# Kernel optimization log

Hardware: AMD Instinct MI355X
Metric: run time of the kernel (lower is better)

## Reference

```python
import jax, jax.numpy as jnp
import numpy as np

B, D, H, E, K = 4096, 1024, 4096, 8, 2

def setup_inputs() -> dict:
    key = jax.random.key(0)
    ks = jax.random.split(key, 6)
    return {
        "x_modality": jax.random.normal(ks[0], (B, D), dtype=jnp.float32),
        "expert_indices": jax.random.randint(ks[1], (B, K), 0, E, dtype=jnp.int32),
        "hard_weights": jax.random.uniform(ks[2], (B, K), dtype=jnp.float32),
        "w1": jax.random.normal(ks[3], (E, D, H), dtype=jnp.float32) * (1.0 / np.sqrt(D)),
        "b1": jnp.zeros((E, H), dtype=jnp.float32),
        "w2": jax.random.normal(ks[4], (E, H, D), dtype=jnp.float32) * (1.0 / np.sqrt(H)),
        "b2": jnp.zeros((E, D), dtype=jnp.float32),
    }

def reference(x_modality, expert_indices, hard_weights, w1, b1, w2, b2):
    b = x_modality.shape[0]
    # Per-token gate per expert: sum of hard_weights over top_k slots routed to that expert.
    gates = jnp.zeros((b, E), dtype=x_modality.dtype)
    gates = gates.at[jnp.arange(b)[:, None], expert_indices].add(hard_weights)  # [b, E]
    # Dense expert compute (small fixed E), then gated combine.
    h = jax.nn.gelu(jnp.einsum("bd,edh->ebh", x_modality, w1) + b1[:, None, :], approximate=False)
    y = jnp.einsum("ebh,ehd->ebd", h, w2) + b2[:, None, :]  # [E, b, D]
    return jnp.einsum("be,ebd->bd", gates, y)
```

## Files before the change

### kernel.cpp

```cpp
#include <hip/hip_runtime.h>
#include <hip/hip_bf16.h>
#include <math.h>

#define NB 4096
#define ND 1024
#define NH 4096
#define NE 8
#define NKK 2
#define NROWS (NB*NKK)
#define MAXT2 40

typedef __attribute__((ext_vector_type(8))) short short8;
typedef __attribute__((ext_vector_type(4))) float f32x4;

__device__ __forceinline__ void gload_lds16(const void* g, void* l) {
    __builtin_amdgcn_global_load_lds(
        (const __attribute__((address_space(1))) unsigned int*)g,
        (__attribute__((address_space(3))) unsigned int*)l, 16, 0, 0);
}

__device__ __forceinline__ unsigned short f2bf(float f) {
    __hip_bfloat16 h = __float2bfloat16(f);
    return *reinterpret_cast<unsigned short*>(&h);
}

__device__ __forceinline__ float fast_gelu(float x) {
    float xs  = x * 0.70710678118654752f;
    float axs = fabsf(xs);
    float t   = __builtin_amdgcn_rcpf(1.0f + 0.3275911f * axs);
    float p   = t * (0.254829592f + t * (-0.284496736f + t * (1.421413741f +
                t * (-1.453152027f + t * 1.061405429f))));
    float e   = __expf(-xs * xs);
    float erf_abs = 1.0f - p * e;
    float erf = copysignf(erf_abs, x);
    return 0.5f * x * (1.0f + erf);
}


__global__ void k_transpose_cvt(const float* __restrict__ in, __hip_bfloat16* __restrict__ out,
                                int R, int C) {
    __shared__ float tile[64][68];
    const size_t ebase = (size_t)blockIdx.z * R * C;
    const int r0 = blockIdx.y * 64, c0 = blockIdx.x * 64;
    const int t = threadIdx.x;
    const int lr = t >> 4, lc4 = (t & 15) * 4;
    #pragma unroll
    for (int i = 0; i < 4; ++i) {
        int r = lr + i * 16;
        float4 v = *reinterpret_cast<const float4*>(&in[ebase + (size_t)(r0 + r) * C + (c0 + lc4)]);
        *reinterpret_cast<float4*>(&tile[r][lc4]) = v;
    }
    __syncthreads();
    const int q = t & 15, cw = t >> 4;
    #pragma unroll
    for (int i = 0; i < 4; ++i) {
        int cc = cw + i * 16;
        ushort4 v;
        v.x = f2bf(tile[q*4+0][cc]);
        v.y = f2bf(tile[q*4+1][cc]);
        v.z = f2bf(tile[q*4+2][cc]);
        v.w = f2bf(tile[q*4+3][cc]);
        *reinterpret_cast<ushort4*>(&out[ebase + (size_t)(c0 + cc) * R + (r0 + q*4)]) = v;
    }
}


__global__ void k_route_count(const int* __restrict__ idx, int* cnt) {
    int b = blockIdx.x * 256 + threadIdx.x;
    if (b < NB) {
        atomicAdd(&cnt[idx[2*b]], 1);
        atomicAdd(&cnt[idx[2*b+1]], 1);
    }
}

__global__ void k_route_scan(const int* __restrict__ cnt, int* offs, int* cursor,
                             int* tile_e, int* tile_row, int* ntiles) {
    if (threadIdx.x == 0) {
        int s = 0, t = 0;
        for (int e = 0; e < NE; ++e) {
            offs[e] = s; cursor[e] = s;
            for (int r = 0; r < cnt[e]; r += 256) {
                tile_e[t] = e; tile_row[t] = s + r; ++t;
            }
            s += cnt[e];
        }
        offs[NE] = s;
        *ntiles = t;
    }
}

__global__ void k_route_fill(const int* __restrict__ idx, const float* __restrict__ hw,
                             int* cursor, int* tok, float* gw) {
    int b = blockIdx.x * 256 + threadIdx.x;
    if (b < NB) {
        #pragma unroll
        for (int k = 0; k < NKK; ++k) {
            int e = idx[2*b + k];
            int p = atomicAdd(&cursor[e], 1);
            tok[p] = b;
            gw[p]  = hw[2*b + k];
        }
    }
}

__global__ void k_gather_cvt(const float* __restrict__ x, const int* __restrict__ tok,
                             __hip_bfloat16* __restrict__ Ag) {
    const int row = blockIdx.x;
    const float4 v = reinterpret_cast<const float4*>(x + (size_t)tok[row] * ND)[threadIdx.x];
    ushort4 u; u.x = f2bf(v.x); u.y = f2bf(v.y); u.z = f2bf(v.z); u.w = f2bf(v.w);
    reinterpret_cast<ushort4*>(Ag + (size_t)row * ND)[threadIdx.x] = u;
}


template<int STAGE>
__global__ __launch_bounds__(512, 2) void moe_gemm(
    const __hip_bfloat16* __restrict__ Asrc,
    const __hip_bfloat16* __restrict__ Bt,
    const float* __restrict__ bias,
    __hip_bfloat16* __restrict__ Hout,
    float* __restrict__ Out,
    const int* __restrict__ offs,
    const int* __restrict__ tok,
    const float* __restrict__ gw,
    const int* __restrict__ tile_e,
    const int* __restrict__ tile_row,
    const int* __restrict__ ntiles)
{
    constexpr int N   = (STAGE == 1) ? NH : ND;
    constexpr int K   = (STAGE == 1) ? ND : NH;
    constexpr int BN  = (STAGE == 1) ? 256 : 128;
    constexpr int KT  = (STAGE == 1) ? 16 : 32;
    constexpr int NI  = BN / 64;
    constexpr int BR  = (BN * 64) / (512 * 8);
    constexpr int ASZ = 256 * 64;
    constexpr int BUF = ASZ + BN * 64;

    extern __shared__ __hip_bfloat16 smem[];

    const int bid = blockIdx.x;
    const int xcd = bid & 7;
    const int c   = bid >> 3;
    const int tile = (xcd >> 1) * 10 + (c >> 3);
    const int sub  = c & 7;
    if (tile >= *ntiles) return;

    int nt, kbase;
    if (STAGE == 1) { nt = (xcd & 1) * 8 + sub; kbase = 0; }
    else            { nt = sub;                 kbase = (xcd & 1) * (NH / 2); }

    const int e = tile_e[tile];
    const int rowbase = tile_row[tile];
    const int end = offs[e + 1];

    const int tid = threadIdx.x;
    const int w = tid >> 6, l = tid & 63;
    const int srow = tid >> 3;
    const int schunk = (tid & 7) ^ (srow & 7);

    const __hip_bfloat16* aptr[4];
    #pragma unroll
    for (int r = 0; r < 4; ++r) {
        int re = rowbase + srow + r * 64; if (re > end - 1) re = end - 1;
        aptr[r] = Asrc + (size_t)re * K + kbase + schunk * 8;
    }
    const __hip_bfloat16* bptr[BR];
    #pragma unroll
    for (int r = 0; r < BR; ++r)
        bptr[r] = Bt + ((size_t)e * N + (size_t)(nt * BN + srow + r * 64)) * K + kbase + schunk * 8;

    const int wm  = (w >> 2) * 128;
    const int wn  = (w & 3) * (BN / 4);
    const int l15 = l & 15, l4 = l >> 4;

    const int cs[2] = { ((l4) ^ (l15 & 7)) * 16, ((4 + l4) ^ (l15 & 7)) * 16 };
    const int abase = (wm + l15) * 128;
    const int bbase = (wn + l15) * 128;

    f32x4 acc[8][NI];
    #pragma unroll
    for (int mi = 0; mi < 8; ++mi)
        #pragma unroll
        for (int ni = 0; ni < NI; ++ni) acc[mi][ni] = (f32x4){0.f, 0.f, 0.f, 0.f};

    auto stage_t = [&](int b, int kt) {
        __hip_bfloat16* da = smem + b * BUF;
        __hip_bfloat16* db = da + ASZ;
        #pragma unroll
        for (int r = 0; r < 4; ++r)  gload_lds16(aptr[r] + kt * 64, da + tid * 8 + r * 4096);
        #pragma unroll
        for (int r = 0; r < BR; ++r) gload_lds16(bptr[r] + kt * 64, db + tid * 8 + r * 4096);
    };

    stage_t(0, 0);
    __syncthreads();

    int cur = 0;
    #pragma unroll 1
    for (int kt = 0; kt < KT; ++kt) {
        if (kt + 1 < KT) stage_t(cur ^ 1, kt + 1);
        const char* sa = (const char*)(smem + cur * BUF);
        const char* sb = (const char*)(smem + cur * BUF + ASZ);
        __builtin_amdgcn_s_setprio(1);
        #pragma unroll
        for (int ks = 0; ks < 2; ++ks) {
            short8 af[8], bfv[NI];
            #pragma unroll
            for (int mi = 0; mi < 8; ++mi)
                af[mi] = *(const short8*)(sa + abase + mi * 2048 + cs[ks]);
            #pragma unroll
            for (int ni = 0; ni < NI; ++ni)
                bfv[ni] = *(const short8*)(sb + bbase + ni * 2048 + cs[ks]);
            #pragma unroll
            for (int mi = 0; mi < 8; ++mi)
                #pragma unroll
                for (int ni = 0; ni < NI; ++ni)
                    acc[mi][ni] = __builtin_amdgcn_mfma_f32_16x16x32_bf16(
                        af[mi], bfv[ni], acc[mi][ni], 0, 0, 0);
        }
        __builtin_amdgcn_s_setprio(0);
        __syncthreads();
        cur ^= 1;
    }

    const int ncol0 = nt * BN + wn;
    #pragma unroll
    for (int mi = 0; mi < 8; ++mi) {
        #pragma unroll
        for (int ni = 0; ni < NI; ++ni) {
            const int gn = ncol0 + ni * 16 + l15;
            const float bv = bias[e * N + gn];
            #pragma unroll
            for (int j = 0; j < 4; ++j) {
                const int re = rowbase + wm + mi * 16 + l4 * 4 + j;
                if (re < end) {
                    float v = acc[mi][ni][j];
                    if (STAGE == 1) {
                        v += bv;
                        Hout[(size_t)re * NH + gn] = __float2bfloat16(fast_gelu(v));
                    } else {
                        if (kbase == 0) v += bv;
                        atomicAdd(&Out[(size_t)tok[re] * ND + gn], gw[re] * v);
                    }
                }
            }
        }
    }
}


extern "C" void kernel_launch(void* const* d_in, const int* in_sizes, int n_in,
                              void* d_out, int out_size, void* d_ws, size_t ws_size,
                              hipStream_t stream) {
    const float* x   = (const float*)d_in[0];
    const int*   idx = (const int*)d_in[1];
    const float* hw  = (const float*)d_in[2];
    const float* w1  = (const float*)d_in[3];
    const float* b1  = (const float*)d_in[4];
    const float* w2  = (const float*)d_in[5];
    const float* b2  = (const float*)d_in[6];
    float* out = (float*)d_out;

    char* ws = (char*)d_ws;
    size_t off = 0;
    __hip_bfloat16* Ag  = (__hip_bfloat16*)(ws + off); off += (size_t)NROWS * ND * 2;
    __hip_bfloat16* w1t = (__hip_bfloat16*)(ws + off); off += (size_t)NE * ND * NH * 2;
    __hip_bfloat16* w2t = (__hip_bfloat16*)(ws + off); off += (size_t)NE * NH * ND * 2;
    __hip_bfloat16* h   = (__hip_bfloat16*)(ws + off); off += (size_t)NROWS * NH * 2;
    int*   tok     = (int*)(ws + off);   off += NROWS * 4;
    float* gwb     = (float*)(ws + off); off += NROWS * 4;
    int*   cnt     = (int*)(ws + off);   off += 16 * 4;
    int*   offs    = (int*)(ws + off);   off += 16 * 4;
    int*   cursor  = (int*)(ws + off);   off += 16 * 4;
    int*   tile_e  = (int*)(ws + off);   off += MAXT2 * 4;
    int*   tile_row= (int*)(ws + off);   off += MAXT2 * 4;
    int*   ntiles  = (int*)(ws + off);   off += 16 * 4;
    (void)ws_size; (void)in_sizes; (void)n_in; (void)out_size;

    hipFuncSetAttribute((const void*)moe_gemm<1>,
                        hipFuncAttributeMaxDynamicSharedMemorySize, 131072);
    hipFuncSetAttribute((const void*)moe_gemm<2>,
                        hipFuncAttributeMaxDynamicSharedMemorySize, 98304);

    hipMemsetAsync(d_out, 0, (size_t)NB * ND * sizeof(float), stream);
    hipMemsetAsync(cnt, 0, 16 * 4, stream);

    k_route_count<<<dim3((NB + 255) / 256), 256, 0, stream>>>(idx, cnt);
    k_route_scan<<<1, 64, 0, stream>>>(cnt, offs, cursor, tile_e, tile_row, ntiles);
    k_route_fill<<<dim3((NB + 255) / 256), 256, 0, stream>>>(idx, hw, cursor, tok, gwb);
    k_gather_cvt<<<dim3(NROWS), 256, 0, stream>>>(x, tok, Ag);
    k_transpose_cvt<<<dim3(NH / 64, ND / 64, NE), 256, 0, stream>>>(w1, w1t, ND, NH);
    k_transpose_cvt<<<dim3(ND / 64, NH / 64, NE), 256, 0, stream>>>(w2, w2t, NH, ND);

    moe_gemm<1><<<dim3(16 * MAXT2), 512, 131072, stream>>>(
        Ag, w1t, b1, h, nullptr, offs, tok, gwb, tile_e, tile_row, ntiles);
    moe_gemm<2><<<dim3(16 * MAXT2), 512, 98304, stream>>>(
        h, w2t, b2, nullptr, out, offs, tok, gwb, tile_e, tile_row, ntiles);
}
```

Before: 492.8 us.

## Shrink MoE GEMM row tiles to 128 and add two-stage prefetch pipeline

Routing tiles are cut from 256 to 128 rows and each wave now computes a 64x64 block. Stage 2 runs with 256 threads and less shared memory, and the grid is remapped to cover up to 72 tiles. The K loop now prefetches two tiles ahead using explicit vmcnt waits and raw barriers. The aim is more blocks in flight, less padded work on partial expert tiles, and better hiding of load latency. The trade-off is more weight reloads per row and more blocks to schedule.

```diff
diff --git a/kernel.cpp b/kernel.cpp
--- a/kernel.cpp
+++ b/kernel.cpp
@@ -8,7 +8,7 @@
 #define NE 8
 #define NKK 2
 #define NROWS (NB*NKK)
-#define MAXT2 40
+#define MAXT 72
 
 typedef __attribute__((ext_vector_type(8))) short short8;
 typedef __attribute__((ext_vector_type(4))) float f32x4;
@@ -79,7 +79,7 @@
         int s = 0, t = 0;
         for (int e = 0; e < NE; ++e) {
             offs[e] = s; cursor[e] = s;
-            for (int r = 0; r < cnt[e]; r += 256) {
+            for (int r = 0; r < cnt[e]; r += 128) {
                 tile_e[t] = e; tile_row[t] = s + r; ++t;
             }
             s += cnt[e];
@@ -113,7 +113,7 @@
 
 
 template<int STAGE>
-__global__ __launch_bounds__(512, 2) void moe_gemm(
+__global__ __launch_bounds__((STAGE == 1) ? 512 : 256, 2) void moe_gemm(
     const __hip_bfloat16* __restrict__ Asrc,
     const __hip_bfloat16* __restrict__ Bt,
     const float* __restrict__ bias,
@@ -126,22 +126,23 @@
     const int* __restrict__ tile_row,
     const int* __restrict__ ntiles)
 {
-    constexpr int N   = (STAGE == 1) ? NH : ND;
-    constexpr int K   = (STAGE == 1) ? ND : NH;
-    constexpr int BN  = (STAGE == 1) ? 256 : 128;
-    constexpr int KT  = (STAGE == 1) ? 16 : 32;
-    constexpr int NI  = BN / 64;
-    constexpr int BR  = (BN * 64) / (512 * 8);
-    constexpr int ASZ = 256 * 64;
-    constexpr int BUF = ASZ + BN * 64;
+    constexpr int N    = (STAGE == 1) ? NH : ND;
+    constexpr int KROW = (STAGE == 1) ? ND : NH;
+    constexpr int KT   = (STAGE == 1) ? 16 : 32;
+    constexpr int BN   = (STAGE == 1) ? 256 : 128;
+    constexpr int THREADS = (STAGE == 1) ? 512 : 256;
+    constexpr int ALr  = (128 * 64) / (THREADS * 8);
+    constexpr int BLr  = (BN * 64) / (THREADS * 8);
+    constexpr int ATS  = 128 * 64;
+    constexpr int BUF  = ATS + BN * 64;
 
     extern __shared__ __hip_bfloat16 smem[];
 
     const int bid = blockIdx.x;
     const int xcd = bid & 7;
     const int c   = bid >> 3;
-    const int tile = (xcd >> 1) * 10 + (c >> 3);
-    const int sub  = c & 7;
+    const int tile = (xcd >> 1) * 18 + (c % 18);
+    const int sub  = c / 18;
     if (tile >= *ntiles) return;
 
     int nt, kbase;
@@ -157,81 +158,101 @@
     const int srow = tid >> 3;
     const int schunk = (tid & 7) ^ (srow & 7);
 
-    const __hip_bfloat16* aptr[4];
-    #pragma unroll
-    for (int r = 0; r < 4; ++r) {
-        int re = rowbase + srow + r * 64; if (re > end - 1) re = end - 1;
-        aptr[r] = Asrc + (size_t)re * K + kbase + schunk * 8;
-    }
-    const __hip_bfloat16* bptr[BR];
-    #pragma unroll
-    for (int r = 0; r < BR; ++r)
-        bptr[r] = Bt + ((size_t)e * N + (size_t)(nt * BN + srow + r * 64)) * K + kbase + schunk * 8;
-
-    const int wm  = (w >> 2) * 128;
-    const int wn  = (w & 3) * (BN / 4);
+    const __hip_bfloat16* aptr[ALr];
+    #pragma unroll
+    for (int r = 0; r < ALr; ++r) {
+        int re = rowbase + srow + r * (THREADS / 8);
+        if (re > end - 1) re = end - 1;
+        aptr[r] = Asrc + (size_t)re * KROW + kbase + schunk * 8;
+    }
+    const __hip_bfloat16* bptr[BLr];
+    #pragma unroll
+    for (int r = 0; r < BLr; ++r)
+        bptr[r] = Bt + ((size_t)e * N + (size_t)(nt * BN + srow + r * (THREADS / 8))) * KROW
+                  + kbase + schunk * 8;
+
+    const int wm = (STAGE == 1) ? (w >> 2) : (w >> 1);
+    const int wn = (STAGE == 1) ? (w & 3)  : (w & 1);
     const int l15 = l & 15, l4 = l >> 4;
 
     const int cs[2] = { ((l4) ^ (l15 & 7)) * 16, ((4 + l4) ^ (l15 & 7)) * 16 };
-    const int abase = (wm + l15) * 128;
-    const int bbase = (wn + l15) * 128;
-
-    f32x4 acc[8][NI];
-    #pragma unroll
-    for (int mi = 0; mi < 8; ++mi)
-        #pragma unroll
-        for (int ni = 0; ni < NI; ++ni) acc[mi][ni] = (f32x4){0.f, 0.f, 0.f, 0.f};
+    const int abase = (wm * 64 + l15) * 128;
+    const int bbase = (wn * 64 + l15) * 128;
+
+    f32x4 acc[4][4];
+    #pragma unroll
+    for (int mi = 0; mi < 4; ++mi)
+        #pragma unroll
+        for (int ni = 0; ni < 4; ++ni) acc[mi][ni] = (f32x4){0.f, 0.f, 0.f, 0.f};
 
     auto stage_t = [&](int b, int kt) {
         __hip_bfloat16* da = smem + b * BUF;
-        __hip_bfloat16* db = da + ASZ;
-        #pragma unroll
-        for (int r = 0; r < 4; ++r)  gload_lds16(aptr[r] + kt * 64, da + tid * 8 + r * 4096);
-        #pragma unroll
-        for (int r = 0; r < BR; ++r) gload_lds16(bptr[r] + kt * 64, db + tid * 8 + r * 4096);
+        __hip_bfloat16* db = da + ATS;
+        #pragma unroll
+        for (int r = 0; r < ALr; ++r)
+            gload_lds16(aptr[r] + kt * 64, da + tid * 8 + r * THREADS * 8);
+        #pragma unroll
+        for (int r = 0; r < BLr; ++r)
+            gload_lds16(bptr[r] + kt * 64, db + tid * 8 + r * THREADS * 8);
     };
 
+    #define WAIT_VM_TILE() do { \
+        if constexpr (STAGE == 1) asm volatile("s_waitcnt vmcnt(6)" ::: "memory"); \
+        else                      asm volatile("s_waitcnt vmcnt(8)" ::: "memory"); } while (0)
+
     stage_t(0, 0);
-    __syncthreads();
-
-    int cur = 0;
+    stage_t(1, 1);
+    WAIT_VM_TILE();
+    __builtin_amdgcn_s_barrier();
+    __builtin_amdgcn_sched_barrier(0);
+
     #pragma unroll 1
     for (int kt = 0; kt < KT; ++kt) {
-        if (kt + 1 < KT) stage_t(cur ^ 1, kt + 1);
+        const int cur = kt & 1;
         const char* sa = (const char*)(smem + cur * BUF);
-        const char* sb = (const char*)(smem + cur * BUF + ASZ);
-        __builtin_amdgcn_s_setprio(1);
-        #pragma unroll
-        for (int ks = 0; ks < 2; ++ks) {
-            short8 af[8], bfv[NI];
+        const char* sb = (const char*)(smem + cur * BUF + ATS);
+        short8 af[4][2], bfv[4][2];
+        #pragma unroll
+        for (int mi = 0; mi < 4; ++mi)
             #pragma unroll
-            for (int mi = 0; mi < 8; ++mi)
-                af[mi] = *(const short8*)(sa + abase + mi * 2048 + cs[ks]);
+            for (int ks = 0; ks < 2; ++ks)
+                af[mi][ks] = *(const short8*)(sa + abase + mi * 2048 + cs[ks]);
+        #pragma unroll
+        for (int ni = 0; ni < 4; ++ni)
             #pragma unroll
-            for (int ni = 0; ni < NI; ++ni)
-                bfv[ni] = *(const short8*)(sb + bbase + ni * 2048 + cs[ks]);
+            for (int ks = 0; ks < 2; ++ks)
+                bfv[ni][ks] = *(const short8*)(sb + bbase + ni * 2048 + cs[ks]);
+        #pragma unroll
+        for (int mi = 0; mi < 4; ++mi)
             #pragma unroll
-            for (int mi = 0; mi < 8; ++mi)
+            for (int ni = 0; ni < 4; ++ni)
                 #pragma unroll
-                for (int ni = 0; ni < NI; ++ni)
+                for (int ks = 0; ks < 2; ++ks)
                     acc[mi][ni] = __builtin_amdgcn_mfma_f32_16x16x32_bf16(
-                        af[mi], bfv[ni], acc[mi][ni], 0, 0, 0);
+                        af[mi][ks], bfv[ni][ks], acc[mi][ni], 0, 0, 0);
+
+        __builtin_amdgcn_s_barrier();
+        __builtin_amdgcn_sched_barrier(0);
+        if (kt + 2 < KT) stage_t(cur, kt + 2);
+        if (kt + 1 < KT) {
+            if (kt + 2 < KT) WAIT_VM_TILE();
+            else             asm volatile("s_waitcnt vmcnt(0)" ::: "memory");
+            __builtin_amdgcn_s_barrier();
+            __builtin_amdgcn_sched_barrier(0);
         }
-        __builtin_amdgcn_s_setprio(0);
-        __syncthreads();
-        cur ^= 1;
-    }
-
-    const int ncol0 = nt * BN + wn;
-    #pragma unroll
-    for (int mi = 0; mi < 8; ++mi) {
-        #pragma unroll
-        for (int ni = 0; ni < NI; ++ni) {
+    }
+    #undef WAIT_VM_TILE
+
+    const int ncol0 = nt * BN + wn * 64;
+    #pragma unroll
+    for (int mi = 0; mi < 4; ++mi) {
+        #pragma unroll
+        for (int ni = 0; ni < 4; ++ni) {
             const int gn = ncol0 + ni * 16 + l15;
             const float bv = bias[e * N + gn];
             #pragma unroll
             for (int j = 0; j < 4; ++j) {
-                const int re = rowbase + wm + mi * 16 + l4 * 4 + j;
+                const int re = rowbase + wm * 64 + mi * 16 + l4 * 4 + j;
                 if (re < end) {
                     float v = acc[mi][ni][j];
                     if (STAGE == 1) {
@@ -271,15 +292,15 @@
     int*   cnt     = (int*)(ws + off);   off += 16 * 4;
     int*   offs    = (int*)(ws + off);   off += 16 * 4;
     int*   cursor  = (int*)(ws + off);   off += 16 * 4;
-    int*   tile_e  = (int*)(ws + off);   off += MAXT2 * 4;
-    int*   tile_row= (int*)(ws + off);   off += MAXT2 * 4;
+    int*   tile_e  = (int*)(ws + off);   off += MAXT * 4;
+    int*   tile_row= (int*)(ws + off);   off += MAXT * 4;
     int*   ntiles  = (int*)(ws + off);   off += 16 * 4;
     (void)ws_size; (void)in_sizes; (void)n_in; (void)out_size;
 
     hipFuncSetAttribute((const void*)moe_gemm<1>,
-                        hipFuncAttributeMaxDynamicSharedMemorySize, 131072);
+                        hipFuncAttributeMaxDynamicSharedMemorySize, 98304);
     hipFuncSetAttribute((const void*)moe_gemm<2>,
-                        hipFuncAttributeMaxDynamicSharedMemorySize, 98304);
+                        hipFuncAttributeMaxDynamicSharedMemorySize, 65536);
 
     hipMemsetAsync(d_out, 0, (size_t)NB * ND * sizeof(float), stream);
     hipMemsetAsync(cnt, 0, 16 * 4, stream);
@@ -291,8 +312,8 @@
     k_transpose_cvt<<<dim3(NH / 64, ND / 64, NE), 256, 0, stream>>>(w1, w1t, ND, NH);
     k_transpose_cvt<<<dim3(ND / 64, NH / 64, NE), 256, 0, stream>>>(w2, w2t, NH, ND);
 
-    moe_gemm<1><<<dim3(16 * MAXT2), 512, 131072, stream>>>(
+    moe_gemm<1><<<dim3(8 * 144), 512, 98304, stream>>>(
         Ag, w1t, b1, h, nullptr, offs, tok, gwb, tile_e, tile_row, ntiles);
-    moe_gemm<2><<<dim3(16 * MAXT2), 512, 98304, stream>>>(
+    moe_gemm<2><<<dim3(8 * 144), 256, 65536, stream>>>(
         h, w2t, b2, nullptr, out, offs, tok, gwb, tile_e, tile_row, ntiles);
 }
```

Measured after the change: 500.7 us. No clear change (+1.6%).

## Rewrite MoE GEMM mainloop with half-K staging and explicit waitcnt pipelining

Applied to the files above, without the earlier changes.

Restructures the grouped GEMM mainloop so each K tile is staged in two half-K pieces. Explicit vmcnt/lgkmcnt waits, s_barrier and sched_barrier interleave LDS reads, global-to-LDS prefetch and MFMA bursts at a finer grain. Stage 2 now uses 256-wide N tiles with a 4-way K split instead of 128-wide N with a 2-way split, which means more atomic adds into the output. The tile-to-workgroup mapping and the LDS swizzle change, and the launch order moves the w2 transpose between the two GEMMs. The hand-coded wait counts are fragile and could break if the compiler reorders memory operations.

```diff
diff --git a/kernel.cpp b/kernel.cpp
--- a/kernel.cpp
+++ b/kernel.cpp
@@ -113,7 +113,7 @@
 
 
 template<int STAGE>
-__global__ __launch_bounds__(512, 2) void moe_gemm(
+__global__ __launch_bounds__(512, 2) void moe_gemm8(
     const __hip_bfloat16* __restrict__ Asrc,
     const __hip_bfloat16* __restrict__ Bt,
     const float* __restrict__ bias,
@@ -126,27 +126,21 @@
     const int* __restrict__ tile_row,
     const int* __restrict__ ntiles)
 {
-    constexpr int N   = (STAGE == 1) ? NH : ND;
-    constexpr int K   = (STAGE == 1) ? ND : NH;
-    constexpr int BN  = (STAGE == 1) ? 256 : 128;
-    constexpr int KT  = (STAGE == 1) ? 16 : 32;
-    constexpr int NI  = BN / 64;
-    constexpr int BR  = (BN * 64) / (512 * 8);
-    constexpr int ASZ = 256 * 64;
-    constexpr int BUF = ASZ + BN * 64;
-
-    extern __shared__ __hip_bfloat16 smem[];
+    constexpr int N    = (STAGE == 1) ? NH : ND;
+    constexpr int KROW = (STAGE == 1) ? ND : NH;
+    constexpr int KT   = 16;
+
+    extern __shared__ char lds[];
 
     const int bid = blockIdx.x;
-    const int xcd = bid & 7;
-    const int c   = bid >> 3;
-    const int tile = (xcd >> 1) * 10 + (c >> 3);
-    const int sub  = c & 7;
+    const int wgid = (bid & 7) * 80 + (bid >> 3);
+    const int tile = wgid % MAXT2;
+    const int rest = wgid / MAXT2;
     if (tile >= *ntiles) return;
 
     int nt, kbase;
-    if (STAGE == 1) { nt = (xcd & 1) * 8 + sub; kbase = 0; }
-    else            { nt = sub;                 kbase = (xcd & 1) * (NH / 2); }
+    if (STAGE == 1) { nt = rest;     kbase = 0; }
+    else            { nt = rest & 3; kbase = (rest >> 2) * (NH / 4); }
 
     const int e = tile_e[tile];
     const int rowbase = tile_row[tile];
@@ -154,86 +148,137 @@
 
     const int tid = threadIdx.x;
     const int w = tid >> 6, l = tid & 63;
-    const int srow = tid >> 3;
-    const int schunk = (tid & 7) ^ (srow & 7);
-
-    const __hip_bfloat16* aptr[4];
-    #pragma unroll
-    for (int r = 0; r < 4; ++r) {
-        int re = rowbase + srow + r * 64; if (re > end - 1) re = end - 1;
-        aptr[r] = Asrc + (size_t)re * K + kbase + schunk * 8;
-    }
-    const __hip_bfloat16* bptr[BR];
-    #pragma unroll
-    for (int r = 0; r < BR; ++r)
-        bptr[r] = Bt + ((size_t)e * N + (size_t)(nt * BN + srow + r * 64)) * K + kbase + schunk * 8;
-
-    const int wm  = (w >> 2) * 128;
-    const int wn  = (w & 3) * (BN / 4);
     const int l15 = l & 15, l4 = l >> 4;
-
-    const int cs[2] = { ((l4) ^ (l15 & 7)) * 16, ((4 + l4) ^ (l15 & 7)) * 16 };
-    const int abase = (wm + l15) * 128;
-    const int bbase = (wn + l15) * 128;
-
-    f32x4 acc[8][NI];
-    #pragma unroll
-    for (int mi = 0; mi < 8; ++mi)
-        #pragma unroll
-        for (int ni = 0; ni < NI; ++ni) acc[mi][ni] = (f32x4){0.f, 0.f, 0.f, 0.f};
-
-    auto stage_t = [&](int b, int kt) {
-        __hip_bfloat16* da = smem + b * BUF;
-        __hip_bfloat16* db = da + ASZ;
-        #pragma unroll
-        for (int r = 0; r < 4; ++r)  gload_lds16(aptr[r] + kt * 64, da + tid * 8 + r * 4096);
-        #pragma unroll
-        for (int r = 0; r < BR; ++r) gload_lds16(bptr[r] + kt * 64, db + tid * 8 + r * 4096);
+    const int wm = (w >> 2) * 128;
+    const int wn = (w & 3) * 64;
+
+    const int srow = tid >> 2;
+    const int j = ((tid & 3) - ((tid >> 3) & 3)) & 3;
+    int ar0 = rowbase + srow;       if (ar0 > end - 1) ar0 = end - 1;
+    int ar1 = rowbase + 128 + srow; if (ar1 > end - 1) ar1 = end - 1;
+    const __hip_bfloat16* ap0 = Asrc + (size_t)ar0 * KROW + kbase + j * 8;
+    const __hip_bfloat16* ap1 = Asrc + (size_t)ar1 * KROW + kbase + j * 8;
+    const __hip_bfloat16* bp0 = Bt + ((size_t)e * N + nt * 256 + srow) * KROW + kbase + j * 8;
+    const __hip_bfloat16* bp1 = Bt + ((size_t)e * N + nt * 256 + 128 + srow) * KROW + kbase + j * 8;
+
+    auto STAGE_H = [&](int buf, int op, int ks, int kt) {
+        char* d = lds + buf * 65536 + op * 32768 + ks * 16384 + tid * 16;
+        const __hip_bfloat16* s0 = (op == 0 ? ap0 : bp0) + kt * 64 + ks * 32;
+        const __hip_bfloat16* s1 = (op == 0 ? ap1 : bp1) + kt * 64 + ks * 32;
+        gload_lds16(s0, d);
+        gload_lds16(s1, d + 8192);
     };
 
-    stage_t(0, 0);
-    __syncthreads();
-
-    int cur = 0;
+    int aoff[8][2], boff[4][2];
+    #pragma unroll
+    for (int m = 0; m < 8; ++m) {
+        int row = wm + m * 16 + l15;
+        #pragma unroll
+        for (int ks = 0; ks < 2; ++ks)
+            aoff[m][ks] = ks * 16384 + row * 64 + (((l4 + (row >> 1)) & 3) * 16);
+    }
+    #pragma unroll
+    for (int n = 0; n < 4; ++n) {
+        int row = wn + n * 16 + l15;
+        #pragma unroll
+        for (int ks = 0; ks < 2; ++ks)
+            boff[n][ks] = 32768 + ks * 16384 + row * 64 + (((l4 + (row >> 1)) & 3) * 16);
+    }
+
+    f32x4 acc[8][4];
+    #pragma unroll
+    for (int m = 0; m < 8; ++m)
+        #pragma unroll
+        for (int n = 0; n < 4; ++n) acc[m][n] = (f32x4){0.f, 0.f, 0.f, 0.f};
+
+    STAGE_H(0, 0, 0, 0); STAGE_H(0, 1, 0, 0);
+    STAGE_H(0, 0, 1, 0); STAGE_H(0, 1, 1, 0);
+
     #pragma unroll 1
-    for (int kt = 0; kt < KT; ++kt) {
-        if (kt + 1 < KT) stage_t(cur ^ 1, kt + 1);
-        const char* sa = (const char*)(smem + cur * BUF);
-        const char* sb = (const char*)(smem + cur * BUF + ASZ);
+    for (int t = 0; t < KT; ++t) {
+        const int buf = t & 1;
+        const char* sb = lds + buf * 65536;
+        const bool notlast = (t + 1 < KT);
+        short8 af[8], b0, b1;
+
+        asm volatile("s_waitcnt vmcnt(4)" ::: "memory");
+        __builtin_amdgcn_sched_barrier(0);
+        __builtin_amdgcn_s_barrier();
+        #pragma unroll
+        for (int m = 0; m < 8; ++m) af[m] = *(const short8*)(sb + aoff[m][0]);
+        b0 = *(const short8*)(sb + boff[0][0]);
+        b1 = *(const short8*)(sb + boff[1][0]);
+        if (notlast) { STAGE_H(buf ^ 1, 0, 0, t + 1); STAGE_H(buf ^ 1, 1, 0, t + 1); }
+        __builtin_amdgcn_s_barrier();
+        asm volatile("s_waitcnt lgkmcnt(0)" ::: "memory");
+        __builtin_amdgcn_sched_barrier(0);
         __builtin_amdgcn_s_setprio(1);
         #pragma unroll
-        for (int ks = 0; ks < 2; ++ks) {
-            short8 af[8], bfv[NI];
-            #pragma unroll
-            for (int mi = 0; mi < 8; ++mi)
-                af[mi] = *(const short8*)(sa + abase + mi * 2048 + cs[ks]);
-            #pragma unroll
-            for (int ni = 0; ni < NI; ++ni)
-                bfv[ni] = *(const short8*)(sb + bbase + ni * 2048 + cs[ks]);
-            #pragma unroll
-            for (int mi = 0; mi < 8; ++mi)
-                #pragma unroll
-                for (int ni = 0; ni < NI; ++ni)
-                    acc[mi][ni] = __builtin_amdgcn_mfma_f32_16x16x32_bf16(
-                        af[mi], bfv[ni], acc[mi][ni], 0, 0, 0);
+        for (int m = 0; m < 8; ++m) {
+            acc[m][0] = __builtin_amdgcn_mfma_f32_16x16x32_bf16(af[m], b0, acc[m][0], 0, 0, 0);
+            acc[m][1] = __builtin_amdgcn_mfma_f32_16x16x32_bf16(af[m], b1, acc[m][1], 0, 0, 0);
         }
         __builtin_amdgcn_s_setprio(0);
-        __syncthreads();
-        cur ^= 1;
-    }
-
-    const int ncol0 = nt * BN + wn;
-    #pragma unroll
-    for (int mi = 0; mi < 8; ++mi) {
-        #pragma unroll
-        for (int ni = 0; ni < NI; ++ni) {
-            const int gn = ncol0 + ni * 16 + l15;
+
+        b0 = *(const short8*)(sb + boff[2][0]);
+        b1 = *(const short8*)(sb + boff[3][0]);
+        if (notlast) { STAGE_H(buf ^ 1, 0, 1, t + 1); STAGE_H(buf ^ 1, 1, 1, t + 1); }
+        __builtin_amdgcn_s_barrier();
+        asm volatile("s_waitcnt lgkmcnt(0)" ::: "memory");
+        __builtin_amdgcn_sched_barrier(0);
+        __builtin_amdgcn_s_setprio(1);
+        #pragma unroll
+        for (int m = 0; m < 8; ++m) {
+            acc[m][2] = __builtin_amdgcn_mfma_f32_16x16x32_bf16(af[m], b0, acc[m][2], 0, 0, 0);
+            acc[m][3] = __builtin_amdgcn_mfma_f32_16x16x32_bf16(af[m], b1, acc[m][3], 0, 0, 0);
+        }
+        __builtin_amdgcn_s_setprio(0);
+
+        if (notlast) asm volatile("s_waitcnt vmcnt(8)" ::: "memory");
+        else         asm volatile("s_waitcnt vmcnt(0)" ::: "memory");
+        __builtin_amdgcn_sched_barrier(0);
+        __builtin_amdgcn_s_barrier();
+        #pragma unroll
+        for (int m = 0; m < 8; ++m) af[m] = *(const short8*)(sb + aoff[m][1]);
+        b0 = *(const short8*)(sb + boff[0][1]);
+        b1 = *(const short8*)(sb + boff[1][1]);
+        __builtin_amdgcn_s_barrier();
+        asm volatile("s_waitcnt lgkmcnt(0)" ::: "memory");
+        __builtin_amdgcn_sched_barrier(0);
+        __builtin_amdgcn_s_setprio(1);
+        #pragma unroll
+        for (int m = 0; m < 8; ++m) {
+            acc[m][0] = __builtin_amdgcn_mfma_f32_16x16x32_bf16(af[m], b0, acc[m][0], 0, 0, 0);
+            acc[m][1] = __builtin_amdgcn_mfma_f32_16x16x32_bf16(af[m], b1, acc[m][1], 0, 0, 0);
+        }
+        __builtin_amdgcn_s_setprio(0);
+
+        b0 = *(const short8*)(sb + boff[2][1]);
+        b1 = *(const short8*)(sb + boff[3][1]);
+        __builtin_amdgcn_s_barrier();
+        asm volatile("s_waitcnt lgkmcnt(0)" ::: "memory");
+        __builtin_amdgcn_sched_barrier(0);
+        __builtin_amdgcn_s_setprio(1);
+        #pragma unroll
+        for (int m = 0; m < 8; ++m) {
+            acc[m][2] = __builtin_amdgcn_mfma_f32_16x16x32_bf16(af[m], b0, acc[m][2], 0, 0, 0);
+            acc[m][3] = __builtin_amdgcn_mfma_f32_16x16x32_bf16(af[m], b1, acc[m][3], 0, 0, 0);
+        }
+        __builtin_amdgcn_s_setprio(0);
+    }
+
+    const int ncol0 = nt * 256 + wn;
+    #pragma unroll
+    for (int m = 0; m < 8; ++m) {
+        #pragma unroll
+        for (int n = 0; n < 4; ++n) {
+            const int gn = ncol0 + n * 16 + l15;
             const float bv = bias[e * N + gn];
             #pragma unroll
-            for (int j = 0; j < 4; ++j) {
-                const int re = rowbase + wm + mi * 16 + l4 * 4 + j;
+            for (int jj = 0; jj < 4; ++jj) {
+                const int re = rowbase + wm + m * 16 + l4 * 4 + jj;
                 if (re < end) {
-                    float v = acc[mi][ni][j];
+                    float v = acc[m][n][jj];
                     if (STAGE == 1) {
                         v += bv;
                         Hout[(size_t)re * NH + gn] = __float2bfloat16(fast_gelu(v));
@@ -276,10 +321,10 @@
     int*   ntiles  = (int*)(ws + off);   off += 16 * 4;
     (void)ws_size; (void)in_sizes; (void)n_in; (void)out_size;
 
-    hipFuncSetAttribute((const void*)moe_gemm<1>,
+    hipFuncSetAttribute((const void*)moe_gemm8<1>,
                         hipFuncAttributeMaxDynamicSharedMemorySize, 131072);
-    hipFuncSetAttribute((const void*)moe_gemm<2>,
-                        hipFuncAttributeMaxDynamicSharedMemorySize, 98304);
+    hipFuncSetAttribute((const void*)moe_gemm8<2>,
+                        hipFuncAttributeMaxDynamicSharedMemorySize, 131072);
 
     hipMemsetAsync(d_out, 0, (size_t)NB * ND * sizeof(float), stream);
     hipMemsetAsync(cnt, 0, 16 * 4, stream);
@@ -288,11 +333,12 @@
     k_route_scan<<<1, 64, 0, stream>>>(cnt, offs, cursor, tile_e, tile_row, ntiles);
     k_route_fill<<<dim3((NB + 255) / 256), 256, 0, stream>>>(idx, hw, cursor, tok, gwb);
     k_gather_cvt<<<dim3(NROWS), 256, 0, stream>>>(x, tok, Ag);
+
     k_transpose_cvt<<<dim3(NH / 64, ND / 64, NE), 256, 0, stream>>>(w1, w1t, ND, NH);
+    moe_gemm8<1><<<dim3(640), 512, 131072, stream>>>(
+        Ag, w1t, b1, h, nullptr, offs, tok, gwb, tile_e, tile_row, ntiles);
+
     k_transpose_cvt<<<dim3(ND / 64, NH / 64, NE), 256, 0, stream>>>(w2, w2t, NH, ND);
-
-    moe_gemm<1><<<dim3(16 * MAXT2), 512, 131072, stream>>>(
-        Ag, w1t, b1, h, nullptr, offs, tok, gwb, tile_e, tile_row, ntiles);
-    moe_gemm<2><<<dim3(16 * MAXT2), 512, 98304, stream>>>(
+    moe_gemm8<2><<<dim3(640), 512, 131072, stream>>>(
         h, w2t, b2, nullptr, out, offs, tok, gwb, tile_e, tile_row, ntiles);
 }
```

After: 556.2 us. 1.13x slower.
